# Optimization experiments

Measured on AMD Instinct MI355X. Metric: run time of the kernel, lower is better.

Reference implementation:

```python
import jax, jax.numpy as jnp
import numpy as np

B, S, D = 2, 2048, 1024  # batch, seq, model_dim
E, K, H = 8, 2, 4096     # experts, top_k, expert hidden
CAP_FACTOR = 1.0


def setup_inputs() -> dict:
    key = jax.random.key(0)
    ks = jax.random.split(key, 6)
    scale_in = 1.0 / np.sqrt(D)
    scale_h = 1.0 / np.sqrt(H)
    return {
        "x": jax.random.normal(ks[0], (B, S, D), jnp.float32),
        "wg": jax.random.normal(ks[1], (D, E), jnp.float32) * scale_in,
        "w1": jax.random.normal(ks[2], (E, D, H), jnp.float32) * scale_in,
        "b1": jnp.zeros((E, H), jnp.float32),
        "w2": jax.random.normal(ks[3], (E, H, D), jnp.float32) * scale_h,
        "b2": jnp.zeros((E, D), jnp.float32),
    }


def _moe_forward(x, wg, w1, b1, w2, b2):
    Bb, Ss, Dd = x.shape
    T = Bb * Ss
    cap = int(K * CAP_FACTOR * ((T + E - 1) // E))  # Tutel capacity rule
    xt = x.reshape(T, Dd)

    # ---- gating ----
    logits = xt @ wg                      # [T, E]
    scores = jax.nn.softmax(logits, axis=-1)
    gates_k, idx_k = jax.lax.top_k(scores, K)  # [T, K]
    # normalize_gate=True: renormalize top-k gates
    gates_k = gates_k / jnp.sum(gates_k, axis=-1, keepdims=True)

    # ---- GShard-style location assignment (slot-major cumsum) ----
    masks = jax.nn.one_hot(idx_k, E, dtype=jnp.int32)           # [T, K, E]
    m = jnp.transpose(masks, (1, 0, 2)).reshape(K * T, E)       # slot-major
    locs_full = jnp.cumsum(m, axis=0) - 1                       # [K*T, E]
    loc = jnp.sum(locs_full * m, axis=-1)                       # [K*T]
    loc = loc.reshape(K, T).T                                   # [T, K]
    valid = (loc < cap).astype(xt.dtype)                        # capacity drop
    loc_c = jnp.clip(loc, 0, cap - 1)

    # ---- dispatch: scatter tokens into [E, cap, D] ----
    contrib = (xt[:, None, :] * valid[:, :, None]).reshape(T * K, Dd)
    disp = jnp.zeros((E, cap, Dd), xt.dtype)
    disp = disp.at[idx_k.reshape(-1), loc_c.reshape(-1)].add(contrib)

    # ---- grouped expert FFN ----
    h = jax.nn.relu(jnp.einsum("ecd,edh->ech", disp, w1) + b1[:, None, :])
    out = jnp.einsum("ech,ehd->ecd", h, w2) + b2[:, None, :]

    # ---- combine (postscore): gather + gate-weighted sum ----
    gathered = out[idx_k, loc_c]                                # [T, K, D]
    y = jnp.einsum("tk,tkd->td", gates_k * valid, gathered)
    return y.reshape(Bb, Ss, Dd)


def reference(x, wg, w1, b1, w2, b2):
    return _moe_forward(x, wg, w1, b1, w2, b2)
```

## Files before the change

### kernel.cpp

```cpp
#include <hip/hip_runtime.h>
#include <stdint.h>

#define NTOK 4096
#define DIM  1024
#define NEXP 8
#define HID  4096
#define CAP  1024

typedef __bf16 bf16x8 __attribute__((ext_vector_type(8)));
typedef float  f32x4  __attribute__((ext_vector_type(4)));

__device__ __forceinline__ unsigned short f2bf(float f) {
  unsigned int u = __float_as_uint(f);
  return (unsigned short)((u + 0x7fffu + ((u >> 16) & 1u)) >> 16);
}

__device__ __forceinline__ float bf2f(unsigned int bits16) {
  return __uint_as_float(bits16 << 16);
}

__device__ __forceinline__ void load_lds16(const void* g, void* l) {
  __builtin_amdgcn_global_load_lds(
      (__attribute__((address_space(1))) void*)g,
      (__attribute__((address_space(3))) void*)l,
      16, 0, 0);
}

__global__ void gating_kernel(const float* __restrict__ x, const float* __restrict__ wg,
                              int* __restrict__ tok_e, float* __restrict__ tok_g) {
  const int t = blockIdx.x;
  const int l = threadIdx.x;
  float acc[NEXP];
#pragma unroll
  for (int e = 0; e < NEXP; ++e) acc[e] = 0.f;

  const float4* x4  = (const float4*)(x + (size_t)t * DIM);
  const float4* wg4 = (const float4*)wg;
#pragma unroll
  for (int i = 0; i < 4; ++i) {
    int dq = i * 64 + l;
    float4 xv = x4[dq];
    float xs[4] = {xv.x, xv.y, xv.z, xv.w};
#pragma unroll
    for (int c = 0; c < 4; ++c) {
      int d = dq * 4 + c;
      float4 wa = wg4[d * 2], wb = wg4[d * 2 + 1];
      acc[0] += xs[c] * wa.x; acc[1] += xs[c] * wa.y;
      acc[2] += xs[c] * wa.z; acc[3] += xs[c] * wa.w;
      acc[4] += xs[c] * wb.x; acc[5] += xs[c] * wb.y;
      acc[6] += xs[c] * wb.z; acc[7] += xs[c] * wb.w;
    }
  }
#pragma unroll
  for (int off = 32; off; off >>= 1)
#pragma unroll
    for (int e = 0; e < NEXP; ++e) acc[e] += __shfl_xor(acc[e], off);

  if (l == 0) {
    float m = acc[0];
#pragma unroll
    for (int e = 1; e < NEXP; ++e) m = fmaxf(m, acc[e]);
    float p[NEXP];
#pragma unroll
    for (int e = 0; e < NEXP; ++e) p[e] = __expf(acc[e] - m);
    int e0 = 0; float b0 = p[0];
#pragma unroll
    for (int e = 1; e < NEXP; ++e) if (p[e] > b0) { b0 = p[e]; e0 = e; }
    int e1 = -1; float b1v = -1.f;
#pragma unroll
    for (int e = 0; e < NEXP; ++e) if (e != e0 && p[e] > b1v) { b1v = p[e]; e1 = e; }
    float inv = 1.f / (b0 + b1v);
    tok_e[2 * t] = e0; tok_e[2 * t + 1] = e1;
    tok_g[2 * t] = b0 * inv; tok_g[2 * t + 1] = b1v * inv;
  }
}

__global__ void scan_kernel(const int* __restrict__ tok_e, int* __restrict__ tok_loc,
                            int* __restrict__ slot_map) {
  const int l = threadIdx.x;
  const unsigned long long below = (1ull << l) - 1ull;
  int base[NEXP];
#pragma unroll
  for (int e = 0; e < NEXP; ++e) base[e] = 0;

  int nxt = tok_e[((0 * 64 + l) & (NTOK - 1)) * 2 + ((0 * 64 + l) >> 12)];
  for (int it = 0; it < 128; ++it) {
    int e = nxt;
    if (it + 1 < 128) {
      int g2 = (it + 1) * 64 + l;
      nxt = tok_e[(g2 & (NTOK - 1)) * 2 + (g2 >> 12)];
    }
    int loc = 0;
#pragma unroll
    for (int ex = 0; ex < NEXP; ++ex) {
      unsigned long long msk = __ballot(e == ex);
      int off = __popcll(msk & below);
      if (e == ex) loc = base[ex] + off;
      base[ex] += __popcll(msk);
    }
    int g = it * 64 + l;
    int k = g >> 12, t = g & (NTOK - 1);
    bool valid = loc < CAP;
    tok_loc[t * 2 + k] = valid ? loc : -1;
    if (valid) slot_map[e * CAP + loc] = t;
  }
#pragma unroll
  for (int ex = 0; ex < NEXP; ++ex) {
    int c = base[ex] < CAP ? base[ex] : CAP;
    for (int i = c + l; i < CAP; i += 64) slot_map[ex * CAP + i] = -1;
  }
}

__global__ void dispatch_kernel(const float* __restrict__ x, const int* __restrict__ slot_map,
                                unsigned short* __restrict__ disp) {
  const int s = blockIdx.x;
  const int tid = threadIdx.x;
  int t = slot_map[s];
  uint2 o;
  if (t >= 0) {
    float4 v = ((const float4*)(x + (size_t)t * DIM))[tid];
    o.x = (unsigned)f2bf(v.x) | ((unsigned)f2bf(v.y) << 16);
    o.y = (unsigned)f2bf(v.z) | ((unsigned)f2bf(v.w) << 16);
  } else {
    o.x = 0u; o.y = 0u;
  }
  ((uint2*)(disp + (size_t)s * DIM))[tid] = o;
}

__global__ void transpose_cvt(const float* __restrict__ in, unsigned short* __restrict__ out,
                              int R, int C) {
  __shared__ float tile[64][65];
  const int e = blockIdx.z;
  const float* inp = in + (size_t)e * R * C;
  unsigned short* outp = out + (size_t)e * R * C;
  const int c0 = blockIdx.x * 64, r0 = blockIdx.y * 64;
  const int t = threadIdx.x;
#pragma unroll
  for (int i = 0; i < 4; ++i) {
    int idx = i * 256 + t;
    int r = idx >> 4, c4 = (idx & 15) * 4;
    float4 v = *(const float4*)(inp + (size_t)(r0 + r) * C + c0 + c4);
    tile[r][c4 + 0] = v.x; tile[r][c4 + 1] = v.y;
    tile[r][c4 + 2] = v.z; tile[r][c4 + 3] = v.w;
  }
  __syncthreads();
#pragma unroll
  for (int i = 0; i < 2; ++i) {
    int idx = i * 256 + t;
    int c = idx >> 3, r8 = (idx & 7) * 8;
    unsigned short s[8];
#pragma unroll
    for (int j = 0; j < 8; ++j) s[j] = f2bf(tile[r8 + j][c]);
    uint4 o;
    o.x = (unsigned)s[0] | ((unsigned)s[1] << 16);
    o.y = (unsigned)s[2] | ((unsigned)s[3] << 16);
    o.z = (unsigned)s[4] | ((unsigned)s[5] << 16);
    o.w = (unsigned)s[6] | ((unsigned)s[7] << 16);
    *(uint4*)(outp + (size_t)(c0 + c) * R + r0 + r8) = o;
  }
}

template <int BM, int BN, bool RELU>
__global__ __launch_bounds__(512)
void gemm8(const unsigned short* __restrict__ A, const unsigned short* __restrict__ B,
           const float* __restrict__ bias, unsigned short* __restrict__ C,
           int N, int K) {
  constexpr int M = 1024;
  constexpr int FR = BM / 64;
  constexpr int FC = BN / 128;
  constexpr int ASLOT = (BM / 2) * 64;
  constexpr int BSLOT = (BN / 2) * 64;
  constexpr int LA = BM / 128;
  constexpr int LB = BN / 128;
  static_assert(LA + LB == 4 || LA + LB == 3, "vmcnt literal");

  extern __shared__ __align__(16) unsigned short smem[];
  unsigned short* As = smem;
  unsigned short* Bs = smem + 4 * ASLOT;

  const int mt = M / BM;
  const int ntn = N / BN;
  const int bid = blockIdx.x;
  const int e = bid / (mt * ntn);
  const int rb = bid - e * mt * ntn;
  const int mtile = rb / ntn;
  const int ntile = rb - mtile * ntn;

  A += (size_t)e * M * K;
  B += (size_t)e * N * K;
  bias += (size_t)e * N;
  C += (size_t)e * M * N;
  const int m0 = mtile * BM;
  const int n0 = ntile * BN;

  const int tid = threadIdx.x;
  const int w = tid >> 6, lane = tid & 63;
  const int wm = w >> 2, wn = w & 3;

  const int srow = lane >> 3;
  const int scol = ((lane & 7) ^ srow) * 8;
  const unsigned short* gA = A + (size_t)(m0 + w * 8 + srow) * K + scol;
  const unsigned short* gB = B + (size_t)(n0 + w * 8 + srow) * K + scol;
  const int lbase = w * 512;

  const int arow0 = wm * (BM / 4) + (lane & 15);
  const int brow0 = wn * (BN / 8) + (lane & 15);
  const int c0 = (((lane >> 4) + 0) ^ (lane & 7)) * 8;
  const int c1 = (((lane >> 4) + 4) ^ (lane & 7)) * 8;

  f32x4 acc[2][2][FR][FC] = {};
  const int nt = K >> 6;

#define STAGE_A(T, MH) do {                                                        \
    const unsigned short* g_ = gA + (size_t)((MH) * (BM / 2)) * K + (size_t)(T) * 64; \
    unsigned short* l_ = &As[(2 * ((T) & 1) + (MH)) * ASLOT + lbase];              \
    _Pragma("unroll")                                                              \
    for (int q_ = 0; q_ < LA; ++q_)                                                \
      load_lds16(g_ + (size_t)q_ * 64 * K, l_ + q_ * 4096);                        \
  } while (0)

#define STAGE_B(T, NH) do {                                                        \
    const unsigned short* g_ = gB + (size_t)((NH) * (BN / 2)) * K + (size_t)(T) * 64; \
    unsigned short* l_ = &Bs[(2 * ((T) & 1) + (NH)) * BSLOT + lbase];              \
    _Pragma("unroll")                                                              \
    for (int q_ = 0; q_ < LB; ++q_)                                                \
      load_lds16(g_ + (size_t)q_ * 64 * K, l_ + q_ * 4096);                        \
  } while (0)

#define WAIT_VMN() do {                                                            \
    if constexpr (LA + LB == 4) asm volatile("s_waitcnt vmcnt(4)" ::: "memory");   \
    else                        asm volatile("s_waitcnt vmcnt(3)" ::: "memory");   \
  } while (0)

#define PHASE(MH, NH, ISVM, ...) do {                                              \
    bf16x8 af[FR][2], bfv[FC][2];                                                  \
    const unsigned short* ab_ = &As[(2 * cur + (MH)) * ASLOT + arow0 * 64];        \
    const unsigned short* bb_ = &Bs[(2 * cur + (NH)) * BSLOT + brow0 * 64];        \
    _Pragma("unroll")                                                              \
    for (int f_ = 0; f_ < FR; ++f_) {                                              \
      af[f_][0] = *(const bf16x8*)(ab_ + f_ * 1024 + c0);                          \
      af[f_][1] = *(const bf16x8*)(ab_ + f_ * 1024 + c1);                          \
    }                                                                              \
    _Pragma("unroll")                                                              \
    for (int f_ = 0; f_ < FC; ++f_) {                                              \
      bfv[f_][0] = *(const bf16x8*)(bb_ + f_ * 1024 + c0);                         \
      bfv[f_][1] = *(const bf16x8*)(bb_ + f_ * 1024 + c1);                         \
    }                                                                              \
    __VA_ARGS__                                                                    \
    __builtin_amdgcn_s_barrier();                                                  \
    asm volatile("s_waitcnt lgkmcnt(0)" ::: "memory");                             \
    __builtin_amdgcn_sched_barrier(0);                                             \
    __builtin_amdgcn_s_setprio(1);                                                 \
    _Pragma("unroll")                                                              \
    for (int f_ = 0; f_ < FR; ++f_)                                                \
      _Pragma("unroll")                                                            \
      for (int g_ = 0; g_ < FC; ++g_) {                                            \
        acc[MH][NH][f_][g_] = __builtin_amdgcn_mfma_f32_16x16x32_bf16(             \
            af[f_][0], bfv[g_][0], acc[MH][NH][f_][g_], 0, 0, 0);                  \
        acc[MH][NH][f_][g_] = __builtin_amdgcn_mfma_f32_16x16x32_bf16(             \
            af[f_][1], bfv[g_][1], acc[MH][NH][f_][g_], 0, 0, 0);                  \
      }                                                                            \
    __builtin_amdgcn_s_setprio(0);                                                 \
    if (ISVM) WAIT_VMN();                                                          \
    asm volatile("" ::: "memory");                                                 \
    __builtin_amdgcn_s_barrier();                                                  \
  } while (0)

  STAGE_A(0, 0); STAGE_A(0, 1); STAGE_B(0, 0); STAGE_B(0, 1);
  STAGE_B(1, 0); STAGE_A(1, 0);
  WAIT_VMN();
  __builtin_amdgcn_s_barrier();

  for (int t = 0; t < nt; ++t) {
    const int cur = t & 1;
    const bool s1 = (t + 1) < nt, s2 = (t + 2) < nt;
    PHASE(0, 0, false, if (s1) STAGE_A(t + 1, 1); );
    PHASE(1, 0, false, if (s1) STAGE_B(t + 1, 1); );
    PHASE(0, 1, false, if (s2) STAGE_B(t + 2, 0); );
    PHASE(1, 1, true,  if (s2) STAGE_A(t + 2, 0); );
  }

#undef PHASE
#undef WAIT_VMN
#undef STAGE_B
#undef STAGE_A

  const int lc = lane & 15, quad = lane >> 4;
  constexpr int SW = BN + 8;
  unsigned short* scr = smem;
#pragma unroll
  for (int Mh = 0; Mh < 2; ++Mh) {
    __syncthreads();
#pragma unroll
    for (int Nh = 0; Nh < 2; ++Nh)
#pragma unroll
      for (int f = 0; f < FR; ++f)
#pragma unroll
        for (int g = 0; g < FC; ++g) {
          float bv = bias[n0 + Nh * (BN / 2) + wn * (BN / 8) + g * 16 + lc];
#pragma unroll
          for (int r2 = 0; r2 < 4; ++r2) {
            float v = acc[Mh][Nh][f][g][r2] + bv;
            if (RELU) v = fmaxf(v, 0.f);
            scr[(wm * (BM / 4) + f * 16 + quad * 4 + r2) * SW +
                Nh * (BN / 2) + wn * (BN / 8) + g * 16 + lc] = f2bf(v);
          }
        }
    __syncthreads();
#pragma unroll
    for (int it = 0; it < (BM / 2) * (BN / 8) / 512; ++it) {
      const int u = it * 512 + tid;
      const int row = u / (BN / 8), seg = u % (BN / 8);
      uint4 v = *(const uint4*)&scr[row * SW + seg * 8];
      *(uint4*)&C[(size_t)(m0 + Mh * (BM / 2) + row) * N + n0 + seg * 8] = v;
    }
  }
}

__global__ void combine_kernel(const unsigned short* __restrict__ outb,
                               const int* __restrict__ tok_e, const int* __restrict__ tok_loc,
                               const float* __restrict__ tok_g, float* __restrict__ y) {
  const int t = blockIdx.x;
  const int tid = threadIdx.x;
  int e0 = tok_e[2 * t], e1 = tok_e[2 * t + 1];
  int l0 = tok_loc[2 * t], l1 = tok_loc[2 * t + 1];
  float g0 = tok_g[2 * t], g1 = tok_g[2 * t + 1];
  float ax = 0.f, ay = 0.f, az = 0.f, aw = 0.f;
  if (l0 >= 0) {
    uint2 u = ((const uint2*)(outb + ((size_t)e0 * CAP + l0) * DIM))[tid];
    ax += g0 * bf2f(u.x & 0xffffu); ay += g0 * __uint_as_float(u.x & 0xffff0000u);
    az += g0 * bf2f(u.y & 0xffffu); aw += g0 * __uint_as_float(u.y & 0xffff0000u);
  }
  if (l1 >= 0) {
    uint2 u = ((const uint2*)(outb + ((size_t)e1 * CAP + l1) * DIM))[tid];
    ax += g1 * bf2f(u.x & 0xffffu); ay += g1 * __uint_as_float(u.x & 0xffff0000u);
    az += g1 * bf2f(u.y & 0xffffu); aw += g1 * __uint_as_float(u.y & 0xffff0000u);
  }
  float4 o; o.x = ax; o.y = ay; o.z = az; o.w = aw;
  ((float4*)(y + (size_t)t * DIM))[tid] = o;
}

extern "C" void kernel_launch(void* const* d_in, const int* in_sizes, int n_in,
                              void* d_out, int out_size, void* d_ws, size_t ws_size,
                              hipStream_t stream) {
  const float* x  = (const float*)d_in[0];
  const float* wg = (const float*)d_in[1];
  const float* w1 = (const float*)d_in[2];
  const float* b1 = (const float*)d_in[3];
  const float* w2 = (const float*)d_in[4];
  const float* b2 = (const float*)d_in[5];
  float* y = (float*)d_out;

  char* ws = (char*)d_ws;
  int*   tok_e    = (int*)(ws);
  int*   tok_loc  = (int*)(ws + 32768);
  float* tok_g    = (float*)(ws + 65536);
  int*   slot_map = (int*)(ws + 98304);
  unsigned short* disp = (unsigned short*)(ws + 131072);
  unsigned short* wbuf = (unsigned short*)(ws + 131072 + (16ull << 20));
  unsigned short* h    = (unsigned short*)(ws + 131072 + (80ull << 20));
  unsigned short* outb = (unsigned short*)(ws + 131072 + (144ull << 20));

  static int att = 0;
  if (!att) {
    (void)hipFuncSetAttribute(reinterpret_cast<const void*>(&gemm8<256, 256, true>),
                              hipFuncAttributeMaxDynamicSharedMemorySize, 131072);
    (void)hipFuncSetAttribute(reinterpret_cast<const void*>(&gemm8<128, 256, false>),
                              hipFuncAttributeMaxDynamicSharedMemorySize, 98304);
    att = 1;
  }

  gating_kernel<<<NTOK, 64, 0, stream>>>(x, wg, tok_e, tok_g);
  scan_kernel<<<1, 64, 0, stream>>>(tok_e, tok_loc, slot_map);
  dispatch_kernel<<<NEXP * CAP, 256, 0, stream>>>(x, slot_map, disp);
  transpose_cvt<<<dim3(HID / 64, DIM / 64, NEXP), 256, 0, stream>>>(w1, wbuf, DIM, HID);
  gemm8<256, 256, true><<<NEXP * (1024 / 256) * (HID / 256), 512, 131072, stream>>>(
      disp, wbuf, b1, h, HID, DIM);
  transpose_cvt<<<dim3(DIM / 64, HID / 64, NEXP), 256, 0, stream>>>(w2, wbuf, HID, DIM);
  gemm8<128, 256, false><<<NEXP * (1024 / 128) * (DIM / 256), 512, 98304, stream>>>(
      h, wbuf, b2, outb, DIM, HID);
  combine_kernel<<<NTOK, 256, 0, stream>>>(outb, tok_e, tok_loc, tok_g, y);
}
```

Before: 523.1 us.

## Rewrite expert GEMM with 32x32 MFMA, register-prefetched pipeline, and XCD-aware block remap

Changes the grouped expert GEMM from 16x16x32 to 32x32x16 bf16 MFMA tiles. The main loop now prefetches the next LDS fragments into registers while MFMAs run, with a different staging order and explicit vmcnt waits. Block IDs are remapped so consecutive blocks of one expert land on the same XCD, the launch bound is set to one block per CU, and the weight transpose kernel now handles 128-row tiles per block. The larger MFMA tile is meant to cut LDS read traffic and instruction count, at the cost of many more live registers and a more fragile hand-written wait/barrier schedule.

```diff
diff --git a/kernel.cpp b/kernel.cpp
--- a/kernel.cpp
+++ b/kernel.cpp
@@ -9,6 +9,7 @@
 
 typedef __bf16 bf16x8 __attribute__((ext_vector_type(8)));
 typedef float  f32x4  __attribute__((ext_vector_type(4)));
+typedef float  f32x16 __attribute__((ext_vector_type(16)));
 
 __device__ __forceinline__ unsigned short f2bf(float f) {
   unsigned int u = __float_as_uint(f);
@@ -129,14 +130,14 @@
 
 __global__ void transpose_cvt(const float* __restrict__ in, unsigned short* __restrict__ out,
                               int R, int C) {
-  __shared__ float tile[64][65];
+  __shared__ float tile[128][65];
   const int e = blockIdx.z;
   const float* inp = in + (size_t)e * R * C;
   unsigned short* outp = out + (size_t)e * R * C;
-  const int c0 = blockIdx.x * 64, r0 = blockIdx.y * 64;
+  const int c0 = blockIdx.x * 64, r0 = blockIdx.y * 128;
   const int t = threadIdx.x;
 #pragma unroll
-  for (int i = 0; i < 4; ++i) {
+  for (int i = 0; i < 8; ++i) {
     int idx = i * 256 + t;
     int r = idx >> 4, c4 = (idx & 15) * 4;
     float4 v = *(const float4*)(inp + (size_t)(r0 + r) * C + c0 + c4);
@@ -145,9 +146,9 @@
   }
   __syncthreads();
 #pragma unroll
-  for (int i = 0; i < 2; ++i) {
+  for (int i = 0; i < 4; ++i) {
     int idx = i * 256 + t;
-    int c = idx >> 3, r8 = (idx & 7) * 8;
+    int c = idx >> 4, r8 = (idx & 15) * 8;
     unsigned short s[8];
 #pragma unroll
     for (int j = 0; j < 8; ++j) s[j] = f2bf(tile[r8 + j][c]);
@@ -161,18 +162,17 @@
 }
 
 template <int BM, int BN, bool RELU>
-__global__ __launch_bounds__(512)
+__global__ __launch_bounds__(512, 1)
 void gemm8(const unsigned short* __restrict__ A, const unsigned short* __restrict__ B,
            const float* __restrict__ bias, unsigned short* __restrict__ C,
            int N, int K) {
   constexpr int M = 1024;
-  constexpr int FR = BM / 64;
-  constexpr int FC = BN / 128;
+  constexpr int FR = BM / 128;
   constexpr int ASLOT = (BM / 2) * 64;
   constexpr int BSLOT = (BN / 2) * 64;
   constexpr int LA = BM / 128;
   constexpr int LB = BN / 128;
-  static_assert(LA + LB == 4 || LA + LB == 3, "vmcnt literal");
+  static_assert(BN == 256, "FC==1 layout");
 
   extern __shared__ __align__(16) unsigned short smem[];
   unsigned short* As = smem;
@@ -180,7 +180,9 @@
 
   const int mt = M / BM;
   const int ntn = N / BN;
-  const int bid = blockIdx.x;
+  int bid = blockIdx.x;
+  const int cpx = (int)gridDim.x >> 3;
+  bid = (bid & 7) * cpx + (bid >> 3);
   const int e = bid / (mt * ntn);
   const int rb = bid - e * mt * ntn;
   const int mtile = rb / ntn;
@@ -196,6 +198,9 @@
   const int tid = threadIdx.x;
   const int w = tid >> 6, lane = tid & 63;
   const int wm = w >> 2, wn = w & 3;
+  const int lane32 = lane & 31;
+  const int khalf = lane >> 5;
+  const int fx = lane & 7;
 
   const int srow = lane >> 3;
   const int scol = ((lane & 7) ^ srow) * 8;
@@ -203,109 +208,134 @@
   const unsigned short* gB = B + (size_t)(n0 + w * 8 + srow) * K + scol;
   const int lbase = w * 512;
 
-  const int arow0 = wm * (BM / 4) + (lane & 15);
-  const int brow0 = wn * (BN / 8) + (lane & 15);
-  const int c0 = (((lane >> 4) + 0) ^ (lane & 7)) * 8;
-  const int c1 = (((lane >> 4) + 4) ^ (lane & 7)) * 8;
-
-  f32x4 acc[2][2][FR][FC] = {};
+  int coff[4];
+#pragma unroll
+  for (int ks = 0; ks < 4; ++ks) coff[ks] = ((ks * 2 + khalf) ^ fx) * 8;
+  int aoff[FR];
+#pragma unroll
+  for (int f = 0; f < FR; ++f) aoff[f] = (wm * (FR * 32) + f * 32 + lane32) * 64;
+  const int boff = (wn * 32 + lane32) * 64;
+
+  f32x16 acc[2][2][FR] = {};
+  bf16x8 a0[FR][4], a1[FR][4], b0[4], b1[4];
   const int nt = K >> 6;
 
-#define STAGE_A(T, MH) do {                                                        \
-    const unsigned short* g_ = gA + (size_t)((MH) * (BM / 2)) * K + (size_t)(T) * 64; \
-    unsigned short* l_ = &As[(2 * ((T) & 1) + (MH)) * ASLOT + lbase];              \
-    _Pragma("unroll")                                                              \
-    for (int q_ = 0; q_ < LA; ++q_)                                                \
-      load_lds16(g_ + (size_t)q_ * 64 * K, l_ + q_ * 4096);                        \
-  } while (0)
-
-#define STAGE_B(T, NH) do {                                                        \
-    const unsigned short* g_ = gB + (size_t)((NH) * (BN / 2)) * K + (size_t)(T) * 64; \
-    unsigned short* l_ = &Bs[(2 * ((T) & 1) + (NH)) * BSLOT + lbase];              \
-    _Pragma("unroll")                                                              \
-    for (int q_ = 0; q_ < LB; ++q_)                                                \
-      load_lds16(g_ + (size_t)q_ * 64 * K, l_ + q_ * 4096);                        \
-  } while (0)
-
-#define WAIT_VMN() do {                                                            \
-    if constexpr (LA + LB == 4) asm volatile("s_waitcnt vmcnt(4)" ::: "memory");   \
-    else                        asm volatile("s_waitcnt vmcnt(3)" ::: "memory");   \
-  } while (0)
-
-#define PHASE(MH, NH, ISVM, ...) do {                                              \
-    bf16x8 af[FR][2], bfv[FC][2];                                                  \
-    const unsigned short* ab_ = &As[(2 * cur + (MH)) * ASLOT + arow0 * 64];        \
-    const unsigned short* bb_ = &Bs[(2 * cur + (NH)) * BSLOT + brow0 * 64];        \
-    _Pragma("unroll")                                                              \
-    for (int f_ = 0; f_ < FR; ++f_) {                                              \
-      af[f_][0] = *(const bf16x8*)(ab_ + f_ * 1024 + c0);                          \
-      af[f_][1] = *(const bf16x8*)(ab_ + f_ * 1024 + c1);                          \
-    }                                                                              \
-    _Pragma("unroll")                                                              \
-    for (int f_ = 0; f_ < FC; ++f_) {                                              \
-      bfv[f_][0] = *(const bf16x8*)(bb_ + f_ * 1024 + c0);                         \
-      bfv[f_][1] = *(const bf16x8*)(bb_ + f_ * 1024 + c1);                         \
-    }                                                                              \
-    __VA_ARGS__                                                                    \
-    __builtin_amdgcn_s_barrier();                                                  \
-    asm volatile("s_waitcnt lgkmcnt(0)" ::: "memory");                             \
-    __builtin_amdgcn_sched_barrier(0);                                             \
-    __builtin_amdgcn_s_setprio(1);                                                 \
-    _Pragma("unroll")                                                              \
-    for (int f_ = 0; f_ < FR; ++f_)                                                \
-      _Pragma("unroll")                                                            \
-      for (int g_ = 0; g_ < FC; ++g_) {                                            \
-        acc[MH][NH][f_][g_] = __builtin_amdgcn_mfma_f32_16x16x32_bf16(             \
-            af[f_][0], bfv[g_][0], acc[MH][NH][f_][g_], 0, 0, 0);                  \
-        acc[MH][NH][f_][g_] = __builtin_amdgcn_mfma_f32_16x16x32_bf16(             \
-            af[f_][1], bfv[g_][1], acc[MH][NH][f_][g_], 0, 0, 0);                  \
-      }                                                                            \
-    __builtin_amdgcn_s_setprio(0);                                                 \
-    if (ISVM) WAIT_VMN();                                                          \
-    asm volatile("" ::: "memory");                                                 \
-    __builtin_amdgcn_s_barrier();                                                  \
-  } while (0)
-
-  STAGE_A(0, 0); STAGE_A(0, 1); STAGE_B(0, 0); STAGE_B(0, 1);
-  STAGE_B(1, 0); STAGE_A(1, 0);
-  WAIT_VMN();
-  __builtin_amdgcn_s_barrier();
-
-  for (int t = 0; t < nt; ++t) {
-    const int cur = t & 1;
-    const bool s1 = (t + 1) < nt, s2 = (t + 2) < nt;
-    PHASE(0, 0, false, if (s1) STAGE_A(t + 1, 1); );
-    PHASE(1, 0, false, if (s1) STAGE_B(t + 1, 1); );
-    PHASE(0, 1, false, if (s2) STAGE_B(t + 2, 0); );
-    PHASE(1, 1, true,  if (s2) STAGE_A(t + 2, 0); );
-  }
-
-#undef PHASE
-#undef WAIT_VMN
+#define STAGE_A(T, MH, SLOT)                                                      \
+  { _Pragma("unroll")                                                             \
+    for (int q_ = 0; q_ < LA; ++q_)                                               \
+      load_lds16(gA + (size_t)((MH) * (BM / 2) + q_ * 64) * K + (size_t)(T) * 64, \
+                 &As[(SLOT) * ASLOT + lbase + q_ * 4096]); }
+
+#define STAGE_B(T, NH, SLOT)                                                      \
+  { _Pragma("unroll")                                                             \
+    for (int q_ = 0; q_ < LB; ++q_)                                               \
+      load_lds16(gB + (size_t)((NH) * (BN / 2) + q_ * 64) * K + (size_t)(T) * 64, \
+                 &Bs[(SLOT) * BSLOT + lbase + q_ * 4096]); }
+
+#define READ_A(dst, SLOT)                                                         \
+  { _Pragma("unroll")                                                             \
+    for (int f_ = 0; f_ < FR; ++f_)                                               \
+      _Pragma("unroll")                                                           \
+      for (int k_ = 0; k_ < 4; ++k_)                                              \
+        dst[f_][k_] = *(const bf16x8*)&As[(SLOT) * ASLOT + aoff[f_] + coff[k_]]; }
+
+#define READ_B(dst, SLOT)                                                         \
+  { _Pragma("unroll")                                                             \
+    for (int k_ = 0; k_ < 4; ++k_)                                                \
+      dst[k_] = *(const bf16x8*)&Bs[(SLOT) * BSLOT + boff + coff[k_]]; }
+
+#define MFMA_PH(MH, NH, AARR, BARR)                                               \
+  { __builtin_amdgcn_s_setprio(1);                                               \
+    _Pragma("unroll")                                                             \
+    for (int f_ = 0; f_ < FR; ++f_)                                               \
+      _Pragma("unroll")                                                           \
+      for (int k_ = 0; k_ < 4; ++k_)                                              \
+        acc[MH][NH][f_] = __builtin_amdgcn_mfma_f32_32x32x16_bf16(                \
+            AARR[f_][k_], BARR[k_], acc[MH][NH][f_], 0, 0, 0);                    \
+    __builtin_amdgcn_s_setprio(0); }
+
+#define BARF() { __builtin_amdgcn_s_barrier(); asm volatile("" ::: "memory"); }
+
+#define VMW_PH0(S1)                                                               \
+  { if (S1) { if constexpr (LA == 2) asm volatile("s_waitcnt vmcnt(6)" ::: "memory"); \
+              else                   asm volatile("s_waitcnt vmcnt(5)" ::: "memory"); } \
+    else asm volatile("s_waitcnt vmcnt(0)" ::: "memory"); }
+
+#define VMW_PH2()                                                                 \
+  { if constexpr (LA == 2) asm volatile("s_waitcnt vmcnt(2)" ::: "memory");       \
+    else                   asm volatile("s_waitcnt vmcnt(1)" ::: "memory"); }
+
+#define TILE(T, P)                                                                \
+  {                                                                               \
+    const bool s1_ = (T) + 1 < nt;                                                \
+                                                         \
+    READ_B(b1, 2 * (P) + 1);                                                      \
+    if (s1_) {                                                                    \
+      STAGE_A((T) + 1, 0, 2 * ((P) ^ 1));                                         \
+      STAGE_B((T) + 1, 0, 2 * ((P) ^ 1));                                         \
+      STAGE_B((T) + 1, 1, 2 * ((P) ^ 1) + 1);                                     \
+    }                                                                             \
+    MFMA_PH(0, 0, a0, b0);                                                        \
+    VMW_PH0(s1_);                                                                 \
+    BARF();                                                                       \
+                                                         \
+    READ_A(a1, 2 * (P) + 1);                                                      \
+    MFMA_PH(0, 1, a0, b1);                                                        \
+    BARF();                                                                       \
+                                                         \
+    if (s1_) { STAGE_A((T) + 1, 1, 2 * ((P) ^ 1) + 1); }                          \
+    MFMA_PH(1, 1, a1, b1);                                                        \
+    VMW_PH2();                                                                    \
+    BARF();                                                                       \
+                \
+    if (s1_) { READ_A(a0, 2 * ((P) ^ 1)); }                                       \
+    MFMA_PH(1, 0, a1, b0);                                                        \
+    if (s1_) { READ_B(b0, 2 * ((P) ^ 1)); }                                       \
+    BARF();                                                                       \
+  }
+
+  STAGE_A(0, 0, 0); STAGE_B(0, 0, 0); STAGE_B(0, 1, 1);
+  STAGE_A(0, 1, 1);
+  if constexpr (LA == 2) asm volatile("s_waitcnt vmcnt(2)" ::: "memory");
+  else                   asm volatile("s_waitcnt vmcnt(1)" ::: "memory");
+  BARF();
+  READ_A(a0, 0); READ_B(b0, 0);
+
+  for (int t = 0; t < nt; t += 2) {
+    TILE(t, 0);
+    TILE(t + 1, 1);
+  }
+
+#undef TILE
+#undef VMW_PH2
+#undef VMW_PH0
+#undef BARF
+#undef MFMA_PH
+#undef READ_B
+#undef READ_A
 #undef STAGE_B
 #undef STAGE_A
 
-  const int lc = lane & 15, quad = lane >> 4;
+  asm volatile("s_waitcnt vmcnt(0)" ::: "memory");
   constexpr int SW = BN + 8;
   unsigned short* scr = smem;
+  const int colw = wn * 32 + lane32;
 #pragma unroll
   for (int Mh = 0; Mh < 2; ++Mh) {
     __syncthreads();
 #pragma unroll
-    for (int Nh = 0; Nh < 2; ++Nh)
+    for (int Nh = 0; Nh < 2; ++Nh) {
+      float bv = bias[n0 + Nh * (BN / 2) + colw];
 #pragma unroll
       for (int f = 0; f < FR; ++f)
 #pragma unroll
-        for (int g = 0; g < FC; ++g) {
-          float bv = bias[n0 + Nh * (BN / 2) + wn * (BN / 8) + g * 16 + lc];
-#pragma unroll
-          for (int r2 = 0; r2 < 4; ++r2) {
-            float v = acc[Mh][Nh][f][g][r2] + bv;
-            if (RELU) v = fmaxf(v, 0.f);
-            scr[(wm * (BM / 4) + f * 16 + quad * 4 + r2) * SW +
-                Nh * (BN / 2) + wn * (BN / 8) + g * 16 + lc] = f2bf(v);
-          }
+        for (int r = 0; r < 16; ++r) {
+          int rowin = (r & 3) + 8 * (r >> 2) + 4 * khalf;
+          float v = acc[Mh][Nh][f][r] + bv;
+          if (RELU) v = fmaxf(v, 0.f);
+          scr[(wm * (FR * 32) + f * 32 + rowin) * SW + Nh * (BN / 2) + colw] = f2bf(v);
         }
+    }
     __syncthreads();
 #pragma unroll
     for (int it = 0; it < (BM / 2) * (BN / 8) / 512; ++it) {
@@ -373,10 +403,10 @@
   gating_kernel<<<NTOK, 64, 0, stream>>>(x, wg, tok_e, tok_g);
   scan_kernel<<<1, 64, 0, stream>>>(tok_e, tok_loc, slot_map);
   dispatch_kernel<<<NEXP * CAP, 256, 0, stream>>>(x, slot_map, disp);
-  transpose_cvt<<<dim3(HID / 64, DIM / 64, NEXP), 256, 0, stream>>>(w1, wbuf, DIM, HID);
+  transpose_cvt<<<dim3(HID / 64, DIM / 128, NEXP), 256, 0, stream>>>(w1, wbuf, DIM, HID);
   gemm8<256, 256, true><<<NEXP * (1024 / 256) * (HID / 256), 512, 131072, stream>>>(
       disp, wbuf, b1, h, HID, DIM);
-  transpose_cvt<<<dim3(DIM / 64, HID / 64, NEXP), 256, 0, stream>>>(w2, wbuf, HID, DIM);
+  transpose_cvt<<<dim3(DIM / 64, HID / 128, NEXP), 256, 0, stream>>>(w2, wbuf, HID, DIM);
   gemm8<128, 256, false><<<NEXP * (1024 / 128) * (DIM / 256), 512, 98304, stream>>>(
       h, wbuf, b2, outb, DIM, HID);
   combine_kernel<<<NTOK, 256, 0, stream>>>(outb, tok_e, tok_loc, tok_g, y);
```

New measurement: 522.7 us. No clear change (-0.1%).
